# Performance work log

Measured on AMD Instinct MI355X. Metric: run time of the kernel, lower is better.

## Reference

```python
import jax, jax.numpy as jnp
import numpy as np
import math

B, H, S, D = 4, 16, 2048, 64  # batch, heads, seq, head dim
HEAD_NUM = 64                 # V value dim == Linear in_features
OUT_DIM = 64                  # input4_dim
SCALE = math.sqrt(D)          # scale_factor = sqrt(input3_dim)


def setup_inputs() -> dict:
    key = jax.random.key(0)
    k1, k2, k3, k4, k5 = jax.random.split(key, 5)
    return {
        "q": jax.random.normal(k1, (B, H, S, D), dtype=jnp.float32),
        "k": jax.random.normal(k2, (B, H, S, D), dtype=jnp.float32),
        "v": jax.random.normal(k3, (B, H, S, HEAD_NUM), dtype=jnp.float32),
        "w_out": jax.random.normal(k4, (OUT_DIM, HEAD_NUM), dtype=jnp.float32) * 0.05,
        "b_out": jax.random.normal(k5, (OUT_DIM,), dtype=jnp.float32) * 0.05,
    }


def reference(q, k, v, w_out, b_out):
    # scores = Q K^T / sqrt(d)   -> [B, H, S, S]
    scores = jnp.einsum("bhqd,bhkd->bhqk", q, k) / jnp.float32(SCALE)
    attn = jax.nn.softmax(scores, axis=-1)
    # dropout is identity (eval / p=0)
    y = jnp.einsum("bhqk,bhke->bhqe", attn, v)  # [B, H, S, HEAD_NUM]
    out = jnp.einsum("bhqe,oe->bhqo", y, w_out) + b_out
    return out
```

## Files before the change

### kernel.cpp

```cpp
#include <hip/hip_runtime.h>
#include <math.h>

typedef __attribute__((ext_vector_type(8))) short bf16x8;
typedef __attribute__((ext_vector_type(4))) float f32x4;
typedef __attribute__((ext_vector_type(16))) float f32x16;

#define S_LEN 2048
#define DH 64
#define NHEAD 64
#define HEAD_ELEMS (S_LEN * DH)

#define AS1 __attribute__((address_space(1)))
#define AS3 __attribute__((address_space(3)))

static __device__ __forceinline__ unsigned short f2bf(float f) {
  union { float f; unsigned u; } v; v.f = f;
  return (unsigned short)((v.u + 0x7fffu + ((v.u >> 16) & 1u)) >> 16);
}

static __device__ __forceinline__ void gload16(const void* g, void* l) {
  __builtin_amdgcn_global_load_lds((const AS1 void*)g, (AS3 void*)l, 16, 0, 0);
}

__global__ __launch_bounds__(256)
void prep(const float* __restrict__ k, const float* __restrict__ v,
          unsigned short* __restrict__ ko, unsigned short* __restrict__ vt) {
  __shared__ float t[64][65];
  if (blockIdx.x < 2048) {
    size_t i = ((size_t)blockIdx.x * 256 + threadIdx.x) * 16;
    #pragma unroll
    for (int h = 0; h < 2; ++h) {
      float4 a = *(const float4*)(k + i + h * 8);
      float4 b = *(const float4*)(k + i + h * 8 + 4);
      bf16x8 r;
      r[0]=(short)f2bf(a.x); r[1]=(short)f2bf(a.y); r[2]=(short)f2bf(a.z); r[3]=(short)f2bf(a.w);
      r[4]=(short)f2bf(b.x); r[5]=(short)f2bf(b.y); r[6]=(short)f2bf(b.z); r[7]=(short)f2bf(b.w);
      *(bf16x8*)(ko + i + h * 8) = r;
    }
  } else {
    const int tid  = threadIdx.x;
    const int bi   = blockIdx.x - 2048;
    const int head = bi >> 5;
    const int kc   = bi & 31;
    const float* vp = v + (size_t)head * HEAD_ELEMS + (size_t)kc * 64 * DH;
    #pragma unroll
    for (int i = 0; i < 4; ++i) {
      int fi = tid + i * 256;
      int kk = fi >> 4, e4 = (fi & 15) * 4;
      float4 f = *(const float4*)(vp + kk * DH + e4);
      t[kk][e4] = f.x; t[kk][e4+1] = f.y; t[kk][e4+2] = f.z; t[kk][e4+3] = f.w;
    }
    __syncthreads();
    const int e   = tid >> 2;
    const int kk0 = (tid & 3) * 16;
    unsigned short* vo = vt + (size_t)head * HEAD_ELEMS + (size_t)e * S_LEN + kc * 64 + kk0;
    bf16x8 r;
    #pragma unroll
    for (int j = 0; j < 8; ++j) r[j] = (short)f2bf(t[kk0 + j][e]);
    *(bf16x8*)vo = r;
    #pragma unroll
    for (int j = 0; j < 8; ++j) r[j] = (short)f2bf(t[kk0 + 8 + j][e]);
    *(bf16x8*)(vo + 8) = r;
  }
}

__global__ __launch_bounds__(256, 4)
void attn32(const float* __restrict__ qg, const unsigned short* __restrict__ kb,
            const unsigned short* __restrict__ vtb, const float* __restrict__ wg,
            const float* __restrict__ bg, float* __restrict__ og) {
  __shared__ __align__(16) unsigned short sm[16384];

  const int tid = threadIdx.x;
  const int w   = tid >> 6;
  const int l   = tid & 63;
  const int lq  = l & 31;
  const int hi  = l >> 5;

  const int bxs  = ((blockIdx.x & 7) << 7) | (blockIdx.x >> 3);
  const int bh   = bxs >> 4;
  const int qblk = bxs & 15;

  const unsigned short* kh = kb  + (size_t)bh * HEAD_ELEMS;
  const unsigned short* vh = vtb + (size_t)bh * HEAD_ELEMS;

  bf16x8 qf[4];
  {
    const float QS = 0.125f * 1.44269504f;
    const float* qfp = qg + (size_t)bh * HEAD_ELEMS
                     + (size_t)(qblk * 128 + w * 32 + lq) * DH + hi * 8;
    #pragma unroll
    for (int d = 0; d < 4; ++d) {
      float4 f0 = *(const float4*)(qfp + d * 16);
      float4 f1 = *(const float4*)(qfp + d * 16 + 4);
      bf16x8 a;
      a[0]=(short)f2bf(f0.x*QS); a[1]=(short)f2bf(f0.y*QS);
      a[2]=(short)f2bf(f0.z*QS); a[3]=(short)f2bf(f0.w*QS);
      a[4]=(short)f2bf(f1.x*QS); a[5]=(short)f2bf(f1.y*QS);
      a[6]=(short)f2bf(f1.z*QS); a[7]=(short)f2bf(f1.w*QS);
      qf[d] = a;
    }
  }

  bf16x8 onesv;
  #pragma unroll
  for (int j = 0; j < 8; ++j) onesv[j] = (short)0x3F80;

  const int srow0 = tid >> 3;
  const int scol  = (tid & 7) ^ (srow0 & 7);
  const unsigned short* ks0 = kh + (size_t)srow0 * DH + scol * 8;
  const unsigned short* vs0 = vh + (size_t)srow0 * S_LEN + scol * 8;

  f32x16 yacc0, yacc1, lacc;
  #pragma unroll
  for (int i = 0; i < 16; ++i) { yacc0[i] = 0.f; yacc1[i] = 0.f; lacc[i] = 0.f; }

  {
    char* lb = (char*)sm + (size_t)w * 1024;
    gload16(ks0,                         lb);
    gload16(ks0 + (size_t)32 * DH,       lb + 4096);
    gload16(vs0,                         lb + 8192);
    gload16(vs0 + (size_t)32 * S_LEN,    lb + 12288);
  }
  __syncthreads();

  for (int kt = 0; kt < S_LEN / 64; ++kt) {
    const int b = kt & 1;
    if (kt + 1 < S_LEN / 64) {
      char* lb = (char*)sm + (b ^ 1) * 16384 + (size_t)w * 1024;
      const size_t ko = (size_t)(kt + 1) * 64 * DH;
      const size_t vo = (size_t)(kt + 1) * 64;
      gload16(ks0 + ko,                      lb);
      gload16(ks0 + ko + (size_t)32 * DH,    lb + 4096);
      gload16(vs0 + vo,                      lb + 8192);
      gload16(vs0 + vo + (size_t)32 * S_LEN, lb + 12288);
    }
    const char* K0 = (const char*)sm + b * 16384;
    const char* V0 = K0 + 8192;

    #pragma unroll
    for (int ktile = 0; ktile < 2; ++ktile) {
      f32x16 s;
      #pragma unroll
      for (int i = 0; i < 16; ++i) s[i] = -18.0f;
      {
        const int row = ktile * 32 + lq;
        const int rx  = row & 7;
        #pragma unroll
        for (int d = 0; d < 4; ++d) {
          bf16x8 kf = *(const bf16x8*)(K0 + row * 128 + (((d * 2 + hi) ^ rx) << 4));
          s = __builtin_amdgcn_mfma_f32_32x32x16_bf16(kf, qf[d], s, 0, 0, 0);
        }
      }

      float pe[16];
      #pragma unroll
      for (int i = 0; i < 16; ++i) pe[i] = exp2f(s[i]);

      unsigned pk[8];
      #pragma unroll
      for (int i = 0; i < 8; ++i)
        asm("v_cvt_pk_bf16_f32 %0, %1, %2" : "=v"(pk[i]) : "v"(pe[2 * i]), "v"(pe[2 * i + 1]));
      asm volatile("v_permlane32_swap_b32 %0, %1" : "+v"(pk[0]), "+v"(pk[2]));
      asm volatile("v_permlane32_swap_b32 %0, %1" : "+v"(pk[1]), "+v"(pk[3]));
      asm volatile("v_permlane32_swap_b32 %0, %1" : "+v"(pk[4]), "+v"(pk[6]));
      asm volatile("v_permlane32_swap_b32 %0, %1" : "+v"(pk[5]), "+v"(pk[7]));
      union { unsigned u[4]; bf16x8 v; } f0, f1;
      f0.u[0] = pk[0]; f0.u[1] = pk[1]; f0.u[2] = pk[2]; f0.u[3] = pk[3];
      f1.u[0] = pk[4]; f1.u[1] = pk[5]; f1.u[2] = pk[6]; f1.u[3] = pk[7];

      lacc = __builtin_amdgcn_mfma_f32_32x32x16_bf16(f0.v, onesv, lacc, 0, 0, 0);
      lacc = __builtin_amdgcn_mfma_f32_32x32x16_bf16(f1.v, onesv, lacc, 0, 0, 0);

      {
        const int r0 = lq, r1 = 32 + lq;
        const int rx = lq & 7;
        bf16x8 v00 = *(const bf16x8*)(V0 + r0 * 128 + (((ktile * 4 + 0 + hi) ^ rx) << 4));
        bf16x8 v01 = *(const bf16x8*)(V0 + r0 * 128 + (((ktile * 4 + 2 + hi) ^ rx) << 4));
        bf16x8 v10 = *(const bf16x8*)(V0 + r1 * 128 + (((ktile * 4 + 0 + hi) ^ rx) << 4));
        bf16x8 v11 = *(const bf16x8*)(V0 + r1 * 128 + (((ktile * 4 + 2 + hi) ^ rx) << 4));
        yacc0 = __builtin_amdgcn_mfma_f32_32x32x16_bf16(f0.v, v00, yacc0, 0, 0, 0);
        yacc0 = __builtin_amdgcn_mfma_f32_32x32x16_bf16(f1.v, v01, yacc0, 0, 0, 0);
        yacc1 = __builtin_amdgcn_mfma_f32_32x32x16_bf16(f0.v, v10, yacc1, 0, 0, 0);
        yacc1 = __builtin_amdgcn_mfma_f32_32x32x16_bf16(f1.v, v11, yacc1, 0, 0, 0);
      }
    }
    __syncthreads();
  }

  {
    float inv_[16];
    #pragma unroll
    for (int r = 0; r < 16; ++r) inv_[r] = 1.0f / lacc[r];
    char* Y = (char*)sm + (size_t)w * 4096;
    #pragma unroll
    for (int et = 0; et < 2; ++et) {
      f32x16& ya = et ? yacc1 : yacc0;
      const int e = et * 32 + lq;
      #pragma unroll
      for (int r = 0; r < 16; ++r) {
        const int qr_ = (r & 3) + 8 * (r >> 2) + 4 * hi;
        *(unsigned short*)(Y + qr_ * 128 + (((e >> 3) ^ (qr_ & 7)) << 4) + (e & 7) * 2)
            = f2bf(ya[r] * inv_[r]);
      }
    }
  }
  asm volatile("s_waitcnt lgkmcnt(0)" ::: "memory");
  __builtin_amdgcn_sched_barrier(0);

  f32x16 o0, o1;
  #pragma unroll
  for (int i = 0; i < 16; ++i) { o0[i] = 0.f; o1[i] = 0.f; }
  {
    const char* Y = (const char*)sm + (size_t)w * 4096;
    #pragma unroll
    for (int es = 0; es < 4; ++es) {
      bf16x8 ya = *(const bf16x8*)(Y + lq * 128 + (((es * 2 + hi) ^ (lq & 7)) << 4));
      #pragma unroll
      for (int ot = 0; ot < 2; ++ot) {
        const float* wp = wg + (size_t)(ot * 32 + lq) * 64 + es * 16 + hi * 8;
        float4 w0 = *(const float4*)wp;
        float4 w1 = *(const float4*)(wp + 4);
        bf16x8 wf;
        wf[0]=(short)f2bf(w0.x); wf[1]=(short)f2bf(w0.y); wf[2]=(short)f2bf(w0.z); wf[3]=(short)f2bf(w0.w);
        wf[4]=(short)f2bf(w1.x); wf[5]=(short)f2bf(w1.y); wf[6]=(short)f2bf(w1.z); wf[7]=(short)f2bf(w1.w);
        if (ot == 0) o0 = __builtin_amdgcn_mfma_f32_32x32x16_bf16(ya, wf, o0, 0, 0, 0);
        else         o1 = __builtin_amdgcn_mfma_f32_32x32x16_bf16(ya, wf, o1, 0, 0, 0);
      }
    }
  }
  const float b0 = bg[lq], b1 = bg[32 + lq];
  float* orow = og + (size_t)bh * HEAD_ELEMS + (size_t)(qblk * 128 + w * 32) * DH;
  #pragma unroll
  for (int r = 0; r < 16; ++r) {
    const int qr_ = (r & 3) + 8 * (r >> 2) + 4 * hi;
    orow[qr_ * 64 + lq]      = o0[r] + b0;
    orow[qr_ * 64 + 32 + lq] = o1[r] + b1;
  }
}

static __device__ __forceinline__ int swz(int row, int col) {
  return row * 128 + ((((col >> 3) ^ (row & 7))) << 4) + ((col & 7) << 1);
}

__global__ __launch_bounds__(256, 2)
void attn_proj_kernel(const float* __restrict__ qg, const float* __restrict__ kg,
                      const float* __restrict__ vg, const float* __restrict__ wg,
                      const float* __restrict__ bg, float* __restrict__ og) {
  __shared__ unsigned short lK[64 * 64];
  __shared__ unsigned short lV[64 * 64];
  __shared__ unsigned short lP[4][16 * 64];

  const int tid  = threadIdx.x;
  const int wave = tid >> 6;
  const int lane = tid & 63;
  const int lg   = lane >> 4;
  const int lr   = lane & 15;
  const int bh = blockIdx.x >> 5;
  const int qt = blockIdx.x & 31;
  const size_t head_off = (size_t)bh * S_LEN * 64;
  const float* qp = qg + head_off;
  const float* kp = kg + head_off;
  const float* vp = vg + head_off;

  const int qrow = qt * 64 + wave * 16 + lr;
  bf16x8 qa[2];
  {
    const float* qr = qp + (size_t)qrow * 64 + lg * 8;
    #pragma unroll
    for (int s = 0; s < 2; ++s) {
      float4 f0 = *(const float4*)(qr + s * 32);
      float4 f1 = *(const float4*)(qr + s * 32 + 4);
      bf16x8 a;
      a[0]=(short)f2bf(f0.x*0.125f); a[1]=(short)f2bf(f0.y*0.125f);
      a[2]=(short)f2bf(f0.z*0.125f); a[3]=(short)f2bf(f0.w*0.125f);
      a[4]=(short)f2bf(f1.x*0.125f); a[5]=(short)f2bf(f1.y*0.125f);
      a[6]=(short)f2bf(f1.z*0.125f); a[7]=(short)f2bf(f1.w*0.125f);
      qa[s] = a;
    }
  }
  f32x4 yacc[4];
  #pragma unroll
  for (int e = 0; e < 4; ++e) yacc[e] = (f32x4){0.f, 0.f, 0.f, 0.f};
  float mrow[4], lrow[4];
  #pragma unroll
  for (int r = 0; r < 4; ++r) { mrow[r] = -INFINITY; lrow[r] = 0.f; }

  for (int kt = 0; kt < S_LEN / 64; ++kt) {
    __syncthreads();
    #pragma unroll
    for (int i = 0; i < 4; ++i) {
      int n = tid + i * 256;
      int row = n >> 4;
      int c4 = (n & 15) * 4;
      const size_t goff = (size_t)(kt * 64 + row) * 64 + c4;
      float4 kf = *(const float4*)(kp + goff);
      unsigned p0 = (unsigned)f2bf(kf.x) | ((unsigned)f2bf(kf.y) << 16);
      unsigned p1 = (unsigned)f2bf(kf.z) | ((unsigned)f2bf(kf.w) << 16);
      uint2 pk2; pk2.x = p0; pk2.y = p1;
      *(uint2*)((char*)lK + swz(row, c4)) = pk2;
      float4 vf = *(const float4*)(vp + goff);
      *(unsigned short*)((char*)lV + swz(c4 + 0, row)) = f2bf(vf.x);
      *(unsigned short*)((char*)lV + swz(c4 + 1, row)) = f2bf(vf.y);
      *(unsigned short*)((char*)lV + swz(c4 + 2, row)) = f2bf(vf.z);
      *(unsigned short*)((char*)lV + swz(c4 + 3, row)) = f2bf(vf.w);
    }
    __syncthreads();
    f32x4 sacc[4];
    #pragma unroll
    for (int c = 0; c < 4; ++c) {
      sacc[c] = (f32x4){0.f, 0.f, 0.f, 0.f};
      #pragma unroll
      for (int s = 0; s < 2; ++s) {
        bf16x8 kb2 = *(const bf16x8*)((const char*)lK + swz(c * 16 + lr, s * 32 + lg * 8));
        sacc[c] = __builtin_amdgcn_mfma_f32_16x16x32_bf16(qa[s], kb2, sacc[c], 0, 0, 0);
      }
    }
    float mt[4], alpha[4];
    #pragma unroll
    for (int r = 0; r < 4; ++r) {
      float mm = fmaxf(fmaxf(sacc[0][r], sacc[1][r]), fmaxf(sacc[2][r], sacc[3][r]));
      mm = fmaxf(mm, __shfl_xor(mm, 1));
      mm = fmaxf(mm, __shfl_xor(mm, 2));
      mm = fmaxf(mm, __shfl_xor(mm, 4));
      mm = fmaxf(mm, __shfl_xor(mm, 8));
      mt[r] = fmaxf(mrow[r], mm);
      alpha[r] = __expf(mrow[r] - mt[r]);
      mrow[r] = mt[r];
    }
    #pragma unroll
    for (int c = 0; c < 4; ++c)
      #pragma unroll
      for (int r = 0; r < 4; ++r) sacc[c][r] = __expf(sacc[c][r] - mt[r]);
    #pragma unroll
    for (int r = 0; r < 4; ++r) {
      float sum = sacc[0][r] + sacc[1][r] + sacc[2][r] + sacc[3][r];
      sum += __shfl_xor(sum, 1);
      sum += __shfl_xor(sum, 2);
      sum += __shfl_xor(sum, 4);
      sum += __shfl_xor(sum, 8);
      lrow[r] = lrow[r] * alpha[r] + sum;
      #pragma unroll
      for (int e = 0; e < 4; ++e) yacc[e][r] *= alpha[r];
    }
    unsigned short* pw = lP[wave];
    #pragma unroll
    for (int c = 0; c < 4; ++c)
      #pragma unroll
      for (int r = 0; r < 4; ++r)
        *(unsigned short*)((char*)pw + swz(lg * 4 + r, c * 16 + lr)) = f2bf(sacc[c][r]);
    asm volatile("s_waitcnt lgkmcnt(0)" ::: "memory");
    #pragma unroll
    for (int s = 0; s < 2; ++s) {
      bf16x8 pa = *(const bf16x8*)((const char*)pw + swz(lr, s * 32 + lg * 8));
      #pragma unroll
      for (int e = 0; e < 4; ++e) {
        bf16x8 vb = *(const bf16x8*)((const char*)lV + swz(e * 16 + lr, s * 32 + lg * 8));
        yacc[e] = __builtin_amdgcn_mfma_f32_16x16x32_bf16(pa, vb, yacc[e], 0, 0, 0);
      }
    }
  }
  unsigned short* pw = lP[wave];
  #pragma unroll
  for (int e = 0; e < 4; ++e)
    #pragma unroll
    for (int r = 0; r < 4; ++r)
      *(unsigned short*)((char*)pw + swz(lg * 4 + r, e * 16 + lr)) = f2bf(yacc[e][r] / lrow[r]);
  asm volatile("s_waitcnt lgkmcnt(0)" ::: "memory");
  f32x4 oacc[4];
  #pragma unroll
  for (int c = 0; c < 4; ++c) oacc[c] = (f32x4){0.f, 0.f, 0.f, 0.f};
  #pragma unroll
  for (int s = 0; s < 2; ++s) {
    bf16x8 ya = *(const bf16x8*)((const char*)pw + swz(lr, s * 32 + lg * 8));
    #pragma unroll
    for (int c = 0; c < 4; ++c) {
      const float* wp = wg + (size_t)(c * 16 + lr) * 64 + s * 32 + lg * 8;
      float4 f0 = *(const float4*)wp;
      float4 f1 = *(const float4*)(wp + 4);
      bf16x8 wb;
      wb[0]=(short)f2bf(f0.x); wb[1]=(short)f2bf(f0.y); wb[2]=(short)f2bf(f0.z); wb[3]=(short)f2bf(f0.w);
      wb[4]=(short)f2bf(f1.x); wb[5]=(short)f2bf(f1.y); wb[6]=(short)f2bf(f1.z); wb[7]=(short)f2bf(f1.w);
      oacc[c] = __builtin_amdgcn_mfma_f32_16x16x32_bf16(ya, wb, oacc[c], 0, 0, 0);
    }
  }
  float* op = og + head_off + (size_t)(qt * 64 + wave * 16) * 64;
  #pragma unroll
  for (int c = 0; c < 4; ++c) {
    float bias = bg[c * 16 + lr];
    #pragma unroll
    for (int r = 0; r < 4; ++r)
      op[(size_t)(lg * 4 + r) * 64 + c * 16 + lr] = oacc[c][r] + bias;
  }
}

extern "C" void kernel_launch(void* const* d_in, const int* in_sizes, int n_in,
                              void* d_out, int out_size, void* d_ws, size_t ws_size,
                              hipStream_t stream) {
  const float* q = (const float*)d_in[0];
  const float* k = (const float*)d_in[1];
  const float* v = (const float*)d_in[2];
  const float* w = (const float*)d_in[3];
  const float* b = (const float*)d_in[4];
  float* out = (float*)d_out;

  const size_t tensor_elems = (size_t)NHEAD * HEAD_ELEMS;
  const size_t need = 2ull * tensor_elems * sizeof(unsigned short);

  if (ws_size >= need) {
    unsigned short* kws = (unsigned short*)d_ws;
    unsigned short* vws = kws + tensor_elems;
    prep<<<4096, 256, 0, stream>>>(k, v, kws, vws);
    attn32<<<1024, 256, 0, stream>>>(q, kws, vws, w, b, out);
  } else {
    attn_proj_kernel<<<64 * 32, 256, 0, stream>>>(q, k, v, w, b, out);
  }
}
```

Before: 234.4 us.

## Triple-buffer K/V tiles with 512-thread blocks and raw waitcnt barriers

The attention kernel now uses 8 waves per block, covering 256 queries instead of 128, so every K/V tile loaded into LDS is shared by twice as many queries. The LDS ring grows from two to three buffers, prefetching two tiles ahead, and the per-tile __syncthreads is replaced with explicit s_waitcnt vmcnt plus s_barrier. MFMA groups are wrapped in s_setprio, the score accumulator starts from zero instead of a constant -18 offset, and the row-sum MFMAs move next to the PV MFMAs. The risks are the larger LDS footprint and register pressure: launch_bounds(512,4) may force spills, and LDS use may cap the number of blocks resident per CU.

```diff
diff --git a/kernel.cpp b/kernel.cpp
--- a/kernel.cpp
+++ b/kernel.cpp
@@ -9,6 +9,7 @@
 #define DH 64
 #define NHEAD 64
 #define HEAD_ELEMS (S_LEN * DH)
+#define NT (S_LEN / 64)
 
 #define AS1 __attribute__((address_space(1)))
 #define AS3 __attribute__((address_space(3)))
@@ -64,11 +65,11 @@
   }
 }
 
-__global__ __launch_bounds__(256, 4)
+__global__ __launch_bounds__(512, 4)
 void attn32(const float* __restrict__ qg, const unsigned short* __restrict__ kb,
             const unsigned short* __restrict__ vtb, const float* __restrict__ wg,
             const float* __restrict__ bg, float* __restrict__ og) {
-  __shared__ __align__(16) unsigned short sm[16384];
+  __shared__ __align__(16) unsigned short sm[24576];
 
   const int tid = threadIdx.x;
   const int w   = tid >> 6;
@@ -76,9 +77,9 @@
   const int lq  = l & 31;
   const int hi  = l >> 5;
 
-  const int bxs  = ((blockIdx.x & 7) << 7) | (blockIdx.x >> 3);
-  const int bh   = bxs >> 4;
-  const int qblk = bxs & 15;
+  const int bxs  = ((blockIdx.x & 7) << 6) | (blockIdx.x >> 3);
+  const int bh   = bxs >> 3;
+  const int qblk = bxs & 7;
 
   const unsigned short* kh = kb  + (size_t)bh * HEAD_ELEMS;
   const unsigned short* vh = vtb + (size_t)bh * HEAD_ELEMS;
@@ -87,7 +88,7 @@
   {
     const float QS = 0.125f * 1.44269504f;
     const float* qfp = qg + (size_t)bh * HEAD_ELEMS
-                     + (size_t)(qblk * 128 + w * 32 + lq) * DH + hi * 8;
+                     + (size_t)(qblk * 256 + w * 32 + lq) * DH + hi * 8;
     #pragma unroll
     for (int d = 0; d < 4; ++d) {
       float4 f0 = *(const float4*)(qfp + d * 16);
@@ -105,10 +106,14 @@
   #pragma unroll
   for (int j = 0; j < 8; ++j) onesv[j] = (short)0x3F80;
 
-  const int srow0 = tid >> 3;
-  const int scol  = (tid & 7) ^ (srow0 & 7);
-  const unsigned short* ks0 = kh + (size_t)srow0 * DH + scol * 8;
-  const unsigned short* vs0 = vh + (size_t)srow0 * S_LEN + scol * 8;
+  f32x16 zv;
+  #pragma unroll
+  for (int i = 0; i < 16; ++i) zv[i] = 0.f;
+
+  const int srow = tid >> 3;
+  const int scol = (tid & 7) ^ (srow & 7);
+  const unsigned short* ks0 = kh + (size_t)srow * DH + scol * 8;
+  const unsigned short* vs0 = vh + (size_t)srow * S_LEN + scol * 8;
 
   f32x16 yacc0, yacc1, lacc;
   #pragma unroll
@@ -116,40 +121,42 @@
 
   {
     char* lb = (char*)sm + (size_t)w * 1024;
-    gload16(ks0,                         lb);
-    gload16(ks0 + (size_t)32 * DH,       lb + 4096);
-    gload16(vs0,                         lb + 8192);
-    gload16(vs0 + (size_t)32 * S_LEN,    lb + 12288);
-  }
-  __syncthreads();
-
-  for (int kt = 0; kt < S_LEN / 64; ++kt) {
-    const int b = kt & 1;
-    if (kt + 1 < S_LEN / 64) {
-      char* lb = (char*)sm + (b ^ 1) * 16384 + (size_t)w * 1024;
-      const size_t ko = (size_t)(kt + 1) * 64 * DH;
-      const size_t vo = (size_t)(kt + 1) * 64;
-      gload16(ks0 + ko,                      lb);
-      gload16(ks0 + ko + (size_t)32 * DH,    lb + 4096);
-      gload16(vs0 + vo,                      lb + 8192);
-      gload16(vs0 + vo + (size_t)32 * S_LEN, lb + 12288);
-    }
-    const char* K0 = (const char*)sm + b * 16384;
+    gload16(ks0,                 lb);
+    gload16(vs0,                 lb + 8192);
+    gload16(ks0 + 64 * DH,       lb + 16384);
+    gload16(vs0 + 64,            lb + 16384 + 8192);
+  }
+  asm volatile("s_waitcnt vmcnt(2)" ::: "memory");
+  asm volatile("s_barrier" ::: "memory");
+
+  int cur = 0;
+  for (int kt = 0; kt < NT; ++kt) {
+    if (kt + 2 < NT) {
+      const int pf = (cur == 0) ? 2 : cur - 1;
+      char* lb = (char*)sm + pf * 16384 + (size_t)w * 1024;
+      gload16(ks0 + (size_t)(kt + 2) * 64 * DH, lb);
+      gload16(vs0 + (size_t)(kt + 2) * 64,      lb + 8192);
+    }
+
+    const char* K0 = (const char*)sm + cur * 16384;
     const char* V0 = K0 + 8192;
 
     #pragma unroll
     for (int ktile = 0; ktile < 2; ++ktile) {
       f32x16 s;
-      #pragma unroll
-      for (int i = 0; i < 16; ++i) s[i] = -18.0f;
       {
         const int row = ktile * 32 + lq;
         const int rx  = row & 7;
-        #pragma unroll
-        for (int d = 0; d < 4; ++d) {
-          bf16x8 kf = *(const bf16x8*)(K0 + row * 128 + (((d * 2 + hi) ^ rx) << 4));
-          s = __builtin_amdgcn_mfma_f32_32x32x16_bf16(kf, qf[d], s, 0, 0, 0);
-        }
+        bf16x8 kf0 = *(const bf16x8*)(K0 + row * 128 + (((0 + hi) ^ rx) << 4));
+        bf16x8 kf1 = *(const bf16x8*)(K0 + row * 128 + (((2 + hi) ^ rx) << 4));
+        bf16x8 kf2 = *(const bf16x8*)(K0 + row * 128 + (((4 + hi) ^ rx) << 4));
+        bf16x8 kf3 = *(const bf16x8*)(K0 + row * 128 + (((6 + hi) ^ rx) << 4));
+        __builtin_amdgcn_s_setprio(1);
+        s = __builtin_amdgcn_mfma_f32_32x32x16_bf16(kf0, qf[0], zv, 0, 0, 0);
+        s = __builtin_amdgcn_mfma_f32_32x32x16_bf16(kf1, qf[1], s, 0, 0, 0);
+        s = __builtin_amdgcn_mfma_f32_32x32x16_bf16(kf2, qf[2], s, 0, 0, 0);
+        s = __builtin_amdgcn_mfma_f32_32x32x16_bf16(kf3, qf[3], s, 0, 0, 0);
+        __builtin_amdgcn_s_setprio(0);
       }
 
       float pe[16];
@@ -168,9 +175,6 @@
       f0.u[0] = pk[0]; f0.u[1] = pk[1]; f0.u[2] = pk[2]; f0.u[3] = pk[3];
       f1.u[0] = pk[4]; f1.u[1] = pk[5]; f1.u[2] = pk[6]; f1.u[3] = pk[7];
 
-      lacc = __builtin_amdgcn_mfma_f32_32x32x16_bf16(f0.v, onesv, lacc, 0, 0, 0);
-      lacc = __builtin_amdgcn_mfma_f32_32x32x16_bf16(f1.v, onesv, lacc, 0, 0, 0);
-
       {
         const int r0 = lq, r1 = 32 + lq;
         const int rx = lq & 7;
@@ -178,13 +182,21 @@
         bf16x8 v01 = *(const bf16x8*)(V0 + r0 * 128 + (((ktile * 4 + 2 + hi) ^ rx) << 4));
         bf16x8 v10 = *(const bf16x8*)(V0 + r1 * 128 + (((ktile * 4 + 0 + hi) ^ rx) << 4));
         bf16x8 v11 = *(const bf16x8*)(V0 + r1 * 128 + (((ktile * 4 + 2 + hi) ^ rx) << 4));
+        __builtin_amdgcn_s_setprio(1);
         yacc0 = __builtin_amdgcn_mfma_f32_32x32x16_bf16(f0.v, v00, yacc0, 0, 0, 0);
         yacc0 = __builtin_amdgcn_mfma_f32_32x32x16_bf16(f1.v, v01, yacc0, 0, 0, 0);
         yacc1 = __builtin_amdgcn_mfma_f32_32x32x16_bf16(f0.v, v10, yacc1, 0, 0, 0);
         yacc1 = __builtin_amdgcn_mfma_f32_32x32x16_bf16(f1.v, v11, yacc1, 0, 0, 0);
-      }
-    }
-    __syncthreads();
+        lacc  = __builtin_amdgcn_mfma_f32_32x32x16_bf16(f0.v, onesv, lacc, 0, 0, 0);
+        lacc  = __builtin_amdgcn_mfma_f32_32x32x16_bf16(f1.v, onesv, lacc, 0, 0, 0);
+        __builtin_amdgcn_s_setprio(0);
+      }
+    }
+
+    if (kt + 2 < NT) asm volatile("s_waitcnt vmcnt(2)" ::: "memory");
+    else             asm volatile("s_waitcnt vmcnt(0)" ::: "memory");
+    asm volatile("s_barrier" ::: "memory");
+    cur = (cur == 2) ? 0 : cur + 1;
   }
 
   {
@@ -229,7 +241,7 @@
     }
   }
   const float b0 = bg[lq], b1 = bg[32 + lq];
-  float* orow = og + (size_t)bh * HEAD_ELEMS + (size_t)(qblk * 128 + w * 32) * DH;
+  float* orow = og + (size_t)bh * HEAD_ELEMS + (size_t)(qblk * 256 + w * 32) * DH;
   #pragma unroll
   for (int r = 0; r < 16; ++r) {
     const int qr_ = (r & 3) + 8 * (r >> 2) + 4 * hi;
@@ -410,7 +422,7 @@
     unsigned short* kws = (unsigned short*)d_ws;
     unsigned short* vws = kws + tensor_elems;
     prep<<<4096, 256, 0, stream>>>(k, v, kws, vws);
-    attn32<<<1024, 256, 0, stream>>>(q, kws, vws, w, b, out);
+    attn32<<<512, 512, 0, stream>>>(q, kws, vws, w, b, out);
   } else {
     attn_proj_kernel<<<64 * 32, 256, 0, stream>>>(q, k, v, w, b, out);
   }
```

Result: no change. 232.5 us (-0.8%).

## Pre-swizzle K/V into MFMA fragment layout and load directly to registers

Applied to the files above, without the earlier changes.

The prep kernel now writes K and transposed V in a per-lane MFMA fragment order, so the attention kernel can read operands straight from global memory into registers. This removes the LDS double buffer, the async global-to-LDS copies and the per-tile barriers. The row-sum is now accumulated in scalar registers with a cross-half shuffle instead of an extra MFMA against a ones vector. The kernel also drops the constant -18 score offset and adds s_setprio around the MFMA groups. The cost is that there is no prefetch, so global/L2 latency is exposed per tile and has to be hidden by occupancy. Removing the offset also gives up the guard against exp2 overflow on large scores.

```diff
diff --git a/kernel.cpp b/kernel.cpp
--- a/kernel.cpp
+++ b/kernel.cpp
@@ -9,36 +9,41 @@
 #define DH 64
 #define NHEAD 64
 #define HEAD_ELEMS (S_LEN * DH)
-
-#define AS1 __attribute__((address_space(1)))
-#define AS3 __attribute__((address_space(3)))
+#define NT (S_LEN / 64)
 
 static __device__ __forceinline__ unsigned short f2bf(float f) {
   union { float f; unsigned u; } v; v.f = f;
   return (unsigned short)((v.u + 0x7fffu + ((v.u >> 16) & 1u)) >> 16);
-}
-
-static __device__ __forceinline__ void gload16(const void* g, void* l) {
-  __builtin_amdgcn_global_load_lds((const AS1 void*)g, (AS3 void*)l, 16, 0, 0);
 }
 
 __global__ __launch_bounds__(256)
 void prep(const float* __restrict__ k, const float* __restrict__ v,
           unsigned short* __restrict__ ko, unsigned short* __restrict__ vt) {
   __shared__ float t[64][65];
+  const int tid = threadIdx.x;
   if (blockIdx.x < 2048) {
-    size_t i = ((size_t)blockIdx.x * 256 + threadIdx.x) * 16;
-    #pragma unroll
-    for (int h = 0; h < 2; ++h) {
-      float4 a = *(const float4*)(k + i + h * 8);
-      float4 b = *(const float4*)(k + i + h * 8 + 4);
+    const int head = blockIdx.x >> 5;
+    const int kt   = blockIdx.x & 31;
+    const float* kp = k + (size_t)head * HEAD_ELEMS;
+    unsigned short* kout = ko + (size_t)head * HEAD_ELEMS + (size_t)kt * 4096;
+    #pragma unroll
+    for (int i = 0; i < 2; ++i) {
+      const int c     = i * 256 + tid;
+      const int chunk = c >> 6;
+      const int tt    = chunk >> 2;
+      const int d     = chunk & 3;
+      const int l     = c & 63;
+      const int row   = kt * 64 + tt * 32 + (l & 31);
+      const int col   = d * 16 + (l >> 5) * 8;
+      const float* src = kp + (size_t)row * DH + col;
+      float4 a = *(const float4*)src;
+      float4 b = *(const float4*)(src + 4);
       bf16x8 r;
       r[0]=(short)f2bf(a.x); r[1]=(short)f2bf(a.y); r[2]=(short)f2bf(a.z); r[3]=(short)f2bf(a.w);
       r[4]=(short)f2bf(b.x); r[5]=(short)f2bf(b.y); r[6]=(short)f2bf(b.z); r[7]=(short)f2bf(b.w);
-      *(bf16x8*)(ko + i + h * 8) = r;
+      *(bf16x8*)(kout + (size_t)chunk * 512 + l * 8) = r;
     }
   } else {
-    const int tid  = threadIdx.x;
     const int bi   = blockIdx.x - 2048;
     const int head = bi >> 5;
     const int kc   = bi & 31;
@@ -51,24 +56,31 @@
       t[kk][e4] = f.x; t[kk][e4+1] = f.y; t[kk][e4+2] = f.z; t[kk][e4+3] = f.w;
     }
     __syncthreads();
-    const int e   = tid >> 2;
-    const int kk0 = (tid & 3) * 16;
-    unsigned short* vo = vt + (size_t)head * HEAD_ELEMS + (size_t)e * S_LEN + kc * 64 + kk0;
-    bf16x8 r;
-    #pragma unroll
-    for (int j = 0; j < 8; ++j) r[j] = (short)f2bf(t[kk0 + j][e]);
-    *(bf16x8*)vo = r;
-    #pragma unroll
-    for (int j = 0; j < 8; ++j) r[j] = (short)f2bf(t[kk0 + 8 + j][e]);
-    *(bf16x8*)(vo + 8) = r;
+    unsigned short* vout = vt + (size_t)head * HEAD_ELEMS + (size_t)kc * 4096;
+    #pragma unroll
+    for (int i = 0; i < 2; ++i) {
+      const int c     = i * 256 + tid;
+      const int chunk = c >> 6;
+      const int t2    = chunk >> 2;
+      const int kh    = (chunk >> 1) & 1;
+      const int eh    = chunk & 1;
+      const int l     = c & 63;
+      const int e     = eh * 32 + (l & 31);
+      const int kr    = t2 * 32 + kh * 16 + (l >> 5) * 8;
+      bf16x8 r;
+      #pragma unroll
+      for (int j = 0; j < 8; ++j) r[j] = (short)f2bf(t[kr + j][e]);
+      *(bf16x8*)(vout + (size_t)chunk * 512 + l * 8) = r;
+    }
   }
 }
 
 __global__ __launch_bounds__(256, 4)
-void attn32(const float* __restrict__ qg, const unsigned short* __restrict__ kb,
-            const unsigned short* __restrict__ vtb, const float* __restrict__ wg,
-            const float* __restrict__ bg, float* __restrict__ og) {
-  __shared__ __align__(16) unsigned short sm[16384];
+void attn_reg(const float* __restrict__ qg, const unsigned short* __restrict__ kfb,
+              const unsigned short* __restrict__ vfb, const float* __restrict__ wg,
+              const float* __restrict__ bg, float* __restrict__ og) {
+  __shared__ __align__(16) unsigned short Ylds[4][2048];
+  __shared__ float stats[4][32];
 
   const int tid = threadIdx.x;
   const int w   = tid >> 6;
@@ -80,8 +92,8 @@
   const int bh   = bxs >> 4;
   const int qblk = bxs & 15;
 
-  const unsigned short* kh = kb  + (size_t)bh * HEAD_ELEMS;
-  const unsigned short* vh = vtb + (size_t)bh * HEAD_ELEMS;
+  const unsigned short* kh_ = kfb + (size_t)bh * HEAD_ELEMS + l * 8;
+  const unsigned short* vh_ = vfb + (size_t)bh * HEAD_ELEMS + l * 8;
 
   bf16x8 qf[4];
   {
@@ -101,65 +113,41 @@
     }
   }
 
-  bf16x8 onesv;
-  #pragma unroll
-  for (int j = 0; j < 8; ++j) onesv[j] = (short)0x3F80;
-
-  const int srow0 = tid >> 3;
-  const int scol  = (tid & 7) ^ (srow0 & 7);
-  const unsigned short* ks0 = kh + (size_t)srow0 * DH + scol * 8;
-  const unsigned short* vs0 = vh + (size_t)srow0 * S_LEN + scol * 8;
-
-  f32x16 yacc0, yacc1, lacc;
-  #pragma unroll
-  for (int i = 0; i < 16; ++i) { yacc0[i] = 0.f; yacc1[i] = 0.f; lacc[i] = 0.f; }
-
-  {
-    char* lb = (char*)sm + (size_t)w * 1024;
-    gload16(ks0,                         lb);
-    gload16(ks0 + (size_t)32 * DH,       lb + 4096);
-    gload16(vs0,                         lb + 8192);
-    gload16(vs0 + (size_t)32 * S_LEN,    lb + 12288);
-  }
-  __syncthreads();
-
-  for (int kt = 0; kt < S_LEN / 64; ++kt) {
-    const int b = kt & 1;
-    if (kt + 1 < S_LEN / 64) {
-      char* lb = (char*)sm + (b ^ 1) * 16384 + (size_t)w * 1024;
-      const size_t ko = (size_t)(kt + 1) * 64 * DH;
-      const size_t vo = (size_t)(kt + 1) * 64;
-      gload16(ks0 + ko,                      lb);
-      gload16(ks0 + ko + (size_t)32 * DH,    lb + 4096);
-      gload16(vs0 + vo,                      lb + 8192);
-      gload16(vs0 + vo + (size_t)32 * S_LEN, lb + 12288);
-    }
-    const char* K0 = (const char*)sm + b * 16384;
-    const char* V0 = K0 + 8192;
-
-    #pragma unroll
-    for (int ktile = 0; ktile < 2; ++ktile) {
+  f32x16 yacc0, yacc1, zv;
+  #pragma unroll
+  for (int i = 0; i < 16; ++i) { yacc0[i] = 0.f; yacc1[i] = 0.f; zv[i] = 0.f; }
+  float lsum = 0.f;
+
+  for (int kt = 0; kt < NT; ++kt) {
+    #pragma unroll
+    for (int t = 0; t < 2; ++t) {
+      const unsigned short* kp = kh_ + (size_t)(kt * 8 + t * 4) * 512;
+      const unsigned short* vp = vh_ + (size_t)(kt * 8 + t * 4) * 512;
+      bf16x8 kf0 = *(const bf16x8*)(kp);
+      bf16x8 kf1 = *(const bf16x8*)(kp + 512);
+      bf16x8 kf2 = *(const bf16x8*)(kp + 1024);
+      bf16x8 kf3 = *(const bf16x8*)(kp + 1536);
+      bf16x8 v00 = *(const bf16x8*)(vp);
+      bf16x8 v10 = *(const bf16x8*)(vp + 512);
+      bf16x8 v01 = *(const bf16x8*)(vp + 1024);
+      bf16x8 v11 = *(const bf16x8*)(vp + 1536);
+
       f32x16 s;
-      #pragma unroll
-      for (int i = 0; i < 16; ++i) s[i] = -18.0f;
-      {
-        const int row = ktile * 32 + lq;
-        const int rx  = row & 7;
-        #pragma unroll
-        for (int d = 0; d < 4; ++d) {
-          bf16x8 kf = *(const bf16x8*)(K0 + row * 128 + (((d * 2 + hi) ^ rx) << 4));
-          s = __builtin_amdgcn_mfma_f32_32x32x16_bf16(kf, qf[d], s, 0, 0, 0);
-        }
-      }
-
-      float pe[16];
-      #pragma unroll
-      for (int i = 0; i < 16; ++i) pe[i] = exp2f(s[i]);
+      __builtin_amdgcn_s_setprio(1);
+      s = __builtin_amdgcn_mfma_f32_32x32x16_bf16(kf0, qf[0], zv, 0, 0, 0);
+      s = __builtin_amdgcn_mfma_f32_32x32x16_bf16(kf1, qf[1], s, 0, 0, 0);
+      s = __builtin_amdgcn_mfma_f32_32x32x16_bf16(kf2, qf[2], s, 0, 0, 0);
+      s = __builtin_amdgcn_mfma_f32_32x32x16_bf16(kf3, qf[3], s, 0, 0, 0);
+      __builtin_amdgcn_s_setprio(0);
 
       unsigned pk[8];
       #pragma unroll
-      for (int i = 0; i < 8; ++i)
-        asm("v_cvt_pk_bf16_f32 %0, %1, %2" : "=v"(pk[i]) : "v"(pe[2 * i]), "v"(pe[2 * i + 1]));
+      for (int i = 0; i < 8; ++i) {
+        float a = exp2f(s[2 * i]);
+        float b = exp2f(s[2 * i + 1]);
+        lsum += a + b;
+        asm("v_cvt_pk_bf16_f32 %0, %1, %2" : "=v"(pk[i]) : "v"(a), "v"(b));
+      }
       asm volatile("v_permlane32_swap_b32 %0, %1" : "+v"(pk[0]), "+v"(pk[2]));
       asm volatile("v_permlane32_swap_b32 %0, %1" : "+v"(pk[1]), "+v"(pk[3]));
       asm volatile("v_permlane32_swap_b32 %0, %1" : "+v"(pk[4]), "+v"(pk[6]));
@@ -168,30 +156,22 @@
       f0.u[0] = pk[0]; f0.u[1] = pk[1]; f0.u[2] = pk[2]; f0.u[3] = pk[3];
       f1.u[0] = pk[4]; f1.u[1] = pk[5]; f1.u[2] = pk[6]; f1.u[3] = pk[7];
 
-      lacc = __builtin_amdgcn_mfma_f32_32x32x16_bf16(f0.v, onesv, lacc, 0, 0, 0);
-      lacc = __builtin_amdgcn_mfma_f32_32x32x16_bf16(f1.v, onesv, lacc, 0, 0, 0);
-
-      {
-        const int r0 = lq, r1 = 32 + lq;
-        const int rx = lq & 7;
-        bf16x8 v00 = *(const bf16x8*)(V0 + r0 * 128 + (((ktile * 4 + 0 + hi) ^ rx) << 4));
-        bf16x8 v01 = *(const bf16x8*)(V0 + r0 * 128 + (((ktile * 4 + 2 + hi) ^ rx) << 4));
-        bf16x8 v10 = *(const bf16x8*)(V0 + r1 * 128 + (((ktile * 4 + 0 + hi) ^ rx) << 4));
-        bf16x8 v11 = *(const bf16x8*)(V0 + r1 * 128 + (((ktile * 4 + 2 + hi) ^ rx) << 4));
-        yacc0 = __builtin_amdgcn_mfma_f32_32x32x16_bf16(f0.v, v00, yacc0, 0, 0, 0);
-        yacc0 = __builtin_amdgcn_mfma_f32_32x32x16_bf16(f1.v, v01, yacc0, 0, 0, 0);
-        yacc1 = __builtin_amdgcn_mfma_f32_32x32x16_bf16(f0.v, v10, yacc1, 0, 0, 0);
-        yacc1 = __builtin_amdgcn_mfma_f32_32x32x16_bf16(f1.v, v11, yacc1, 0, 0, 0);
-      }
-    }
-    __syncthreads();
-  }
+      __builtin_amdgcn_s_setprio(1);
+      yacc0 = __builtin_amdgcn_mfma_f32_32x32x16_bf16(f0.v, v00, yacc0, 0, 0, 0);
+      yacc0 = __builtin_amdgcn_mfma_f32_32x32x16_bf16(f1.v, v01, yacc0, 0, 0, 0);
+      yacc1 = __builtin_amdgcn_mfma_f32_32x32x16_bf16(f0.v, v10, yacc1, 0, 0, 0);
+      yacc1 = __builtin_amdgcn_mfma_f32_32x32x16_bf16(f1.v, v11, yacc1, 0, 0, 0);
+      __builtin_amdgcn_s_setprio(0);
+    }
+  }
+
+  lsum += __shfl_xor(lsum, 32);
+  if (hi == 0) stats[w][lq] = 1.0f / lsum;
+  asm volatile("s_waitcnt lgkmcnt(0)" ::: "memory");
+  __builtin_amdgcn_sched_barrier(0);
 
   {
-    float inv_[16];
-    #pragma unroll
-    for (int r = 0; r < 16; ++r) inv_[r] = 1.0f / lacc[r];
-    char* Y = (char*)sm + (size_t)w * 4096;
+    char* Y = (char*)Ylds[w];
     #pragma unroll
     for (int et = 0; et < 2; ++et) {
       f32x16& ya = et ? yacc1 : yacc0;
@@ -200,7 +180,7 @@
       for (int r = 0; r < 16; ++r) {
         const int qr_ = (r & 3) + 8 * (r >> 2) + 4 * hi;
         *(unsigned short*)(Y + qr_ * 128 + (((e >> 3) ^ (qr_ & 7)) << 4) + (e & 7) * 2)
-            = f2bf(ya[r] * inv_[r]);
+            = f2bf(ya[r] * stats[w][qr_]);
       }
     }
   }
@@ -211,7 +191,7 @@
   #pragma unroll
   for (int i = 0; i < 16; ++i) { o0[i] = 0.f; o1[i] = 0.f; }
   {
-    const char* Y = (const char*)sm + (size_t)w * 4096;
+    const char* Y = (const char*)Ylds[w];
     #pragma unroll
     for (int es = 0; es < 4; ++es) {
       bf16x8 ya = *(const bf16x8*)(Y + lq * 128 + (((es * 2 + hi) ^ (lq & 7)) << 4));
@@ -410,7 +390,7 @@
     unsigned short* kws = (unsigned short*)d_ws;
     unsigned short* vws = kws + tensor_elems;
     prep<<<4096, 256, 0, stream>>>(k, v, kws, vws);
-    attn32<<<1024, 256, 0, stream>>>(q, kws, vws, w, b, out);
+    attn_reg<<<1024, 256, 0, stream>>>(q, kws, vws, w, b, out);
   } else {
     attn_proj_kernel<<<64 * 32, 256, 0, stream>>>(q, k, v, w, b, out);
   }
```

After: 236.7 us. About the same (+1.0%).
